# Performance work log

Measured on AMD Instinct MI355X. Metric: run time of the kernel, lower is better.

The kernel has to match this reference:

```python
import jax, jax.numpy as jnp
import numpy as np

D_MODEL = 256
NHEAD = 8
HEAD_DIM = D_MODEL // NHEAD
EPS_ATTN = 1e-6
EPS_LN = 1e-5


def _layernorm(x, g, b):
    mu = jnp.mean(x, axis=-1, keepdims=True)
    var = jnp.mean(jnp.square(x - mu), axis=-1, keepdims=True)
    return (x - mu) * jax.lax.rsqrt(var + EPS_LN) * g + b


def _embed_rotary(t, cos, sin):
    # t, cos, sin: [N, L, C]; interleaved pair rotation as in RoFPE.embed_rotary
    t2 = jnp.stack([-t[..., 1::2], t[..., ::2]], axis=-1).reshape(t.shape)
    return t * cos + t2 * sin


def setup_inputs() -> dict:
    key = jax.random.key(0)
    ks = jax.random.split(key, 12)
    N, L, S, C = 4, 4800, 4800, D_MODEL
    w = lambda k, shp: jax.random.normal(k, shp, dtype=jnp.float32) * 0.05
    return {
        "x": jax.random.normal(ks[0], (N, L, C), dtype=jnp.float32),
        "source": jax.random.normal(ks[1], (N, S, C), dtype=jnp.float32),
        "x_pe": jax.random.normal(ks[2], (N, L, C, 2), dtype=jnp.float32),
        "source_pe": jax.random.normal(ks[3], (N, S, C, 2), dtype=jnp.float32),
        "Wq": w(ks[4], (C, C)),
        "Wk": w(ks[5], (C, C)),
        "Wv": w(ks[6], (C, C)),
        "Wm": w(ks[7], (C, C)),
        "W1": w(ks[8], (2 * C, 2 * C)),
        "W2": w(ks[9], (C, 2 * C)),
        "g1": jnp.ones((C,), dtype=jnp.float32),
        "b1": jnp.zeros((C,), dtype=jnp.float32),
        "g2": jnp.ones((C,), dtype=jnp.float32),
        "b2": jnp.zeros((C,), dtype=jnp.float32),
    }


def reference(x, source, x_pe, source_pe, Wq, Wk, Wv, Wm, W1, W2, g1, b1, g2, b2):
    bs, L, C = x.shape
    H, D = NHEAD, HEAD_DIM
    # projections (nn.Linear: y = x @ W.T)
    q = x @ Wq.T
    k = source @ Wk.T
    v = source @ Wv.T
    # inline rotary PE
    q = _embed_rotary(q, x_pe[..., 0], x_pe[..., 1]).reshape(bs, L, H, D)
    k = _embed_rotary(k, source_pe[..., 0], source_pe[..., 1]).reshape(bs, -1, H, D)
    v = v.reshape(bs, -1, H, D)
    # LoFTR linear attention: phi(x) = elu(x) + 1
    Q = jax.nn.elu(q) + 1.0
    K = jax.nn.elu(k) + 1.0
    v_len = v.shape[1]
    vals = v / v_len
    KV = jnp.einsum("nshd,nshv->nhdv", K, vals)          # [N,H,D,D]
    Z = 1.0 / (jnp.einsum("nlhd,nhd->nlh", Q, K.sum(axis=1)) + EPS_ATTN)
    msg = jnp.einsum("nlhd,nhdv,nlh->nlhv", Q, KV, Z) * v_len  # [N,L,H,D]
    # merge + norm1
    msg = msg.reshape(bs, L, H * D) @ Wm.T
    msg = _layernorm(msg, g1, b1)
    # concat-MLP + norm2 + residual
    h = jnp.concatenate([x, msg], axis=-1)               # [N,L,2C]
    h = jax.nn.relu(h @ W1.T) @ W2.T
    h = _layernorm(h, g2, b2)
    return x + h
```

## Files before the change

### kernel.cpp

```cpp
#include <hip/hip_runtime.h>
#include <hip/hip_bf16.h>
#include <math.h>

#define NROWS 19200
#define SLEN  4800
#define KV_CHUNKS 50
#define KV_SC     96

typedef unsigned short ushort_t;
typedef __attribute__((ext_vector_type(8))) short bf16x8;
typedef __attribute__((ext_vector_type(4))) float f32x4;
typedef __attribute__((ext_vector_type(8))) unsigned short ushort8;

__device__ __forceinline__ float bf2f(ushort_t u) {
  union { unsigned int i; float f; } x; x.i = ((unsigned int)u) << 16; return x.f;
}
__device__ __forceinline__ ushort_t f2bf(float f) {
  __hip_bfloat16 h = __float2bfloat16(f);
  union { __hip_bfloat16 h; ushort_t u; } x; x.h = h; return x.u;
}

#define GLOAD16(g, l) __builtin_amdgcn_global_load_lds( \
    (const __attribute__((address_space(1))) unsigned int*)(g), \
    (__attribute__((address_space(3))) unsigned int*)(l), 16, 0, 0)

template <int EPI, bool CONCAT>
__device__ __forceinline__ void gemmT_body(
    const ushort_t* __restrict__ A0, const ushort_t* __restrict__ A1,
    const ushort_t* __restrict__ W, ushort_t* __restrict__ outp,
    int Nn, int K, int bm, int bn, char* smem) {
  const int tid = threadIdx.x;
  const int wave = tid >> 6, lane = tid & 63;
  const int wm = (wave >> 1) * 64, wn = (wave & 1) * 64;
  const int l15 = lane & 15, l4 = lane >> 4;

  f32x4 acc[4][4];
#pragma unroll
  for (int i = 0; i < 4; ++i)
#pragma unroll
    for (int j = 0; j < 4; ++j) acc[i][j] = (f32x4){0.f, 0.f, 0.f, 0.f};

  for (int k0 = 0; k0 < K; k0 += 64) {
    const ushort_t* Asrc;
    int ka;
    if (CONCAT) { Asrc = (k0 < 256) ? A0 : A1; ka = k0 & 255; }
    else        { Asrc = A0; ka = k0; }
#pragma unroll
    for (int c = 0; c < 4; ++c) {
      int ch = c * 4 + wave;
      int o = ch * 1024 + lane * 16;
      int row = o >> 7, g = (o >> 4) & 7;
      const ushort_t* sp =
          Asrc + (size_t)(bm + row) * 256 + ka + ((g ^ (row & 7)) << 3);
      GLOAD16(sp, smem + ch * 1024);
    }
#pragma unroll
    for (int c = 0; c < 4; ++c) {
      int ch = c * 4 + wave;
      int o = ch * 1024 + lane * 16;
      int row = o >> 7, g = (o >> 4) & 7;
      const ushort_t* sp =
          W + (size_t)(bn + row) * K + k0 + ((g ^ (row & 7)) << 3);
      GLOAD16(sp, smem + 16384 + ch * 1024);
    }
    __syncthreads();
#pragma unroll
    for (int kc = 0; kc < 2; ++kc) {
      bf16x8 af[4], bfr[4];
#pragma unroll
      for (int mi = 0; mi < 4; ++mi) {
        int r = wm + mi * 16 + l15;
        int G = kc * 4 + l4;
        af[mi] = *(const bf16x8*)(smem + r * 128 + ((G ^ (r & 7)) << 4));
      }
#pragma unroll
      for (int ni = 0; ni < 4; ++ni) {
        int r = wn + ni * 16 + l15;
        int G = kc * 4 + l4;
        bfr[ni] = *(const bf16x8*)(smem + 16384 + r * 128 +
                                   ((G ^ (r & 7)) << 4));
      }
#pragma unroll
      for (int mi = 0; mi < 4; ++mi)
#pragma unroll
        for (int ni = 0; ni < 4; ++ni)
          acc[mi][ni] = __builtin_amdgcn_mfma_f32_16x16x32_bf16(
              af[mi], bfr[ni], acc[mi][ni], 0, 0, 0);
    }
    __syncthreads();
  }

  ushort_t* st = (ushort_t*)smem;
#pragma unroll
  for (int mi = 0; mi < 4; ++mi)
#pragma unroll
    for (int ni = 0; ni < 4; ++ni)
#pragma unroll
      for (int j = 0; j < 4; ++j) {
        int trow = wm + mi * 16 + l4 * 4 + j;
        int tcol = wn + ni * 16 + l15;
        float v = acc[mi][ni][j];
        if (EPI == 3) v = fmaxf(v, 0.f);
        st[trow * 140 + tcol] = f2bf(v);
      }
  __syncthreads();
#pragma unroll
  for (int c = 0; c < 8; ++c) {
    int ch = c * 256 + tid;
    int row = ch >> 4, g = ch & 15;
    ushort8 u = *(const ushort8*)&st[row * 140 + g * 8];
    *(ushort8*)&outp[(size_t)(bm + row) * Nn + bn + g * 8] = u;
  }
}

__global__ __launch_bounds__(256) void qkv_fused(
    const ushort_t* __restrict__ xb, const ushort_t* __restrict__ srcb,
    const ushort_t* __restrict__ Wqb, const ushort_t* __restrict__ Wkb,
    const ushort_t* __restrict__ Wvb,
    ushort_t* __restrict__ Q, ushort_t* __restrict__ Kb,
    ushort_t* __restrict__ Vb) {
  extern __shared__ char smem[];
  int b = blockIdx.x;
  const int which = b < 300 ? 0 : (b < 600 ? 1 : 2);
  b -= which * 300;
  const int bm = (b >> 1) * 128, bn = (b & 1) * 128;
  const ushort_t* A = (which == 0) ? xb : srcb;
  const ushort_t* W = (which == 0) ? Wqb : (which == 1 ? Wkb : Wvb);
  ushort_t* o = (which == 0) ? Q : (which == 1 ? Kb : Vb);
  gemmT_body<0, false>(A, nullptr, W, o, 256, 256, bm, bn, smem);
}

__global__ __launch_bounds__(256) void mlp1_kernel(
    const ushort_t* __restrict__ xb, const ushort_t* __restrict__ msgln,
    const ushort_t* __restrict__ W1b, ushort_t* __restrict__ h1) {
  extern __shared__ char smem[];
  const int bm = (blockIdx.x >> 2) * 128, bn = (blockIdx.x & 3) * 128;
  gemmT_body<3, true>(xb, msgln, W1b, h1, 512, 512, bm, bn, smem);
}

template <int KDIM, bool RESID, bool OUTBF>
__global__ __launch_bounds__(256) void gemm_ln_kernel(
    const ushort_t* __restrict__ A, const ushort_t* __restrict__ W,
    const float* __restrict__ g, const float* __restrict__ bb,
    const float* __restrict__ resid, void* __restrict__ outp) {
  __shared__ char As[32 * 128];
  __shared__ char Bs[256 * 128];
  __shared__ float partS[4][32];
  __shared__ float partQ[4][32];
  __shared__ float gS[256], bS[256];

  const int tid = threadIdx.x;
  const int wave = tid >> 6, lane = tid & 63;
  const int l15 = lane & 15, l4 = lane >> 4;
  const int bm = blockIdx.x * 32;

  gS[tid] = g[tid];
  bS[tid] = bb[tid];

  f32x4 acc[2][4];
#pragma unroll
  for (int i = 0; i < 2; ++i)
#pragma unroll
    for (int j = 0; j < 4; ++j) acc[i][j] = (f32x4){0.f, 0.f, 0.f, 0.f};

  for (int k0 = 0; k0 < KDIM; k0 += 64) {
    {
      int row = tid >> 3, gch = tid & 7;
      const ushort_t* src =
          A + (size_t)(bm + row) * KDIM + k0 + ((gch ^ (row & 7)) << 3);
      GLOAD16(src, As + tid * 16);
    }
#pragma unroll
    for (int c = 0; c < 8; ++c) {
      int ch = c * 256 + tid;
      int row = ch >> 3, gch = ch & 7;
      const ushort_t* src =
          W + (size_t)row * KDIM + k0 + ((gch ^ (row & 7)) << 3);
      GLOAD16(src, Bs + ch * 16);
    }
    __syncthreads();
#pragma unroll
    for (int kc = 0; kc < 2; ++kc) {
      bf16x8 af[2], bfr[4];
#pragma unroll
      for (int mi = 0; mi < 2; ++mi) {
        int r = mi * 16 + l15;
        int G = kc * 4 + l4;
        af[mi] = *(const bf16x8*)(As + r * 128 + ((G ^ (r & 7)) << 4));
      }
#pragma unroll
      for (int ni = 0; ni < 4; ++ni) {
        int r = wave * 64 + ni * 16 + l15;
        int G = kc * 4 + l4;
        bfr[ni] = *(const bf16x8*)(Bs + r * 128 + ((G ^ (r & 7)) << 4));
      }
#pragma unroll
      for (int mi = 0; mi < 2; ++mi)
#pragma unroll
        for (int ni = 0; ni < 4; ++ni)
          acc[mi][ni] = __builtin_amdgcn_mfma_f32_16x16x32_bf16(
              af[mi], bfr[ni], acc[mi][ni], 0, 0, 0);
    }
    __syncthreads();
  }

#pragma unroll
  for (int mi = 0; mi < 2; ++mi)
#pragma unroll
    for (int j = 0; j < 4; ++j) {
      float s = acc[mi][0][j] + acc[mi][1][j] + acc[mi][2][j] + acc[mi][3][j];
      float q = acc[mi][0][j] * acc[mi][0][j] + acc[mi][1][j] * acc[mi][1][j] +
                acc[mi][2][j] * acc[mi][2][j] + acc[mi][3][j] * acc[mi][3][j];
#pragma unroll
      for (int m = 1; m < 16; m <<= 1) {
        s += __shfl_xor(s, m);
        q += __shfl_xor(q, m);
      }
      if (l15 == 0) {
        int row = mi * 16 + l4 * 4 + j;
        partS[wave][row] = s;
        partQ[wave][row] = q;
      }
    }
  __syncthreads();

  float mu[2][4], rsv[2][4];
#pragma unroll
  for (int mi = 0; mi < 2; ++mi)
#pragma unroll
    for (int j = 0; j < 4; ++j) {
      int row = mi * 16 + l4 * 4 + j;
      float s = partS[0][row] + partS[1][row] + partS[2][row] + partS[3][row];
      float q2 = partQ[0][row] + partQ[1][row] + partQ[2][row] + partQ[3][row];
      float m_ = s * (1.f / 256.f);
      float var = q2 * (1.f / 256.f) - m_ * m_;
      mu[mi][j] = m_;
      rsv[mi][j] = rsqrtf(var + 1e-5f);
    }

#pragma unroll
  for (int mi = 0; mi < 2; ++mi)
#pragma unroll
    for (int ni = 0; ni < 4; ++ni)
#pragma unroll
      for (int j = 0; j < 4; ++j) {
        int row = mi * 16 + l4 * 4 + j;
        int col = wave * 64 + ni * 16 + l15;
        float v = (acc[mi][ni][j] - mu[mi][j]) * rsv[mi][j] * gS[col] + bS[col];
        size_t gr = (size_t)(bm + row);
        if (RESID) v += resid[gr * 256 + col];
        if (OUTBF)
          ((ushort_t*)outp)[gr * 256 + col] = f2bf(v);
        else
          ((float*)outp)[gr * 256 + col] = v;
      }
}

__global__ __launch_bounds__(256) void kv_partial(
    const ushort_t* __restrict__ Kb, const ushort_t* __restrict__ Vb,
    const float* __restrict__ s_pe,
    float* __restrict__ kvp, float* __restrict__ ksp) {
  __shared__ float bufK[32][32];
  __shared__ float bufV[32][32];
  const int b = blockIdx.x;
  const int ch = b % KV_CHUNKS;
  const int nh = b / KV_CHUNKS;
  const int h = nh & 7, n = nh >> 3;
  const int tid = threadIdx.x;
  const int d = tid >> 3, vb = (tid & 7) * 4;
  const int half = tid >> 7, t = tid & 127;
  const int srow = t >> 2, seg = (t & 3) * 8;
  const int segS = (seg + 8 * (srow & 3)) & 31;
  float a0 = 0.f, a1 = 0.f, a2 = 0.f, a3 = 0.f, ks = 0.f;
  const size_t base = (size_t)n * SLEN * 256 + (size_t)h * 32;
  const int s0 = ch * KV_SC;
  for (int s = s0; s < s0 + KV_SC; s += 32) {
    __syncthreads();
    const size_t eoff = base + (size_t)(s + srow) * 256 + seg;
    ushort8 u = *(const ushort8*)((half ? Vb : Kb) + eoff);
    float v[8];
#pragma unroll
    for (int i = 0; i < 8; ++i) v[i] = bf2f((ushort_t)u[i]);
    if (!half) {
      const float4* pp = (const float4*)&s_pe[eoff * 2];
      float4 p0 = pp[0], p1 = pp[1], p2 = pp[2], p3 = pp[3];
      float r[8];
      r[0] = v[0] * p0.x - v[1] * p0.y; r[1] = v[1] * p0.z + v[0] * p0.w;
      r[2] = v[2] * p1.x - v[3] * p1.y; r[3] = v[3] * p1.z + v[2] * p1.w;
      r[4] = v[4] * p2.x - v[5] * p2.y; r[5] = v[5] * p2.z + v[4] * p2.w;
      r[6] = v[6] * p3.x - v[7] * p3.y; r[7] = v[7] * p3.z + v[6] * p3.w;
#pragma unroll
      for (int i = 0; i < 8; ++i)
        v[i] = r[i] > 0.f ? r[i] + 1.f : __expf(r[i]);
    }
    float* dst = half ? &bufV[srow][segS] : &bufK[srow][segS];
    *(float4*)dst = (float4){v[0], v[1], v[2], v[3]};
    *(float4*)(dst + 4) = (float4){v[4], v[5], v[6], v[7]};
    __syncthreads();
#pragma unroll
    for (int ss = 0; ss < 32; ++ss) {
      int rot = 8 * (ss & 3);
      float kd = bufK[ss][(d + rot) & 31];
      float4 vv = *(const float4*)&bufV[ss][(vb + rot) & 31];
      a0 += kd * vv.x; a1 += kd * vv.y; a2 += kd * vv.z; a3 += kd * vv.w;
      ks += kd;
    }
  }
  float* kv = &kvp[(size_t)b * 1024 + d * 32 + vb];
  kv[0] = a0; kv[1] = a1; kv[2] = a2; kv[3] = a3;
  if ((tid & 7) == 0) ksp[(size_t)b * 32 + d] = ks;
}

__global__ __launch_bounds__(256) void kv_reduce(
    const float* __restrict__ kvp, const float* __restrict__ ksp,
    float* __restrict__ KV, float* __restrict__ Ksum) {
  const int nh = blockIdx.x;
  const int tid = threadIdx.x;
  for (int e = tid; e < 1024; e += 256) {
    float s = 0.f;
    for (int p = 0; p < KV_CHUNKS; ++p)
      s += kvp[(size_t)(nh * KV_CHUNKS + p) * 1024 + e];
    KV[(size_t)nh * 1024 + e] = s;
  }
  if (tid < 32) {
    float s = 0.f;
    for (int p = 0; p < KV_CHUNKS; ++p)
      s += ksp[(size_t)(nh * KV_CHUNKS + p) * 32 + tid];
    Ksum[nh * 32 + tid] = s;
  }
}

__global__ __launch_bounds__(256) void msg_kernel(
    const ushort_t* __restrict__ Qb, const float* __restrict__ x_pe,
    const float* __restrict__ KV, const float* __restrict__ Ksum,
    ushort_t* __restrict__ msg) {
  __shared__ float Qs[8][256];
  __shared__ float Ks[8][32];
  const int b = blockIdx.x;
  const int r0 = b * 8;
  const int n = r0 / SLEN;
  const int tid = threadIdx.x;
  Ks[tid >> 5][tid & 31] = Ksum[(n * 8 + (tid >> 5)) * 32 + (tid & 31)];
  {
    int rr = tid >> 5, cc = (tid & 31) * 8;
    const size_t eoff = (size_t)(r0 + rr) * 256 + cc;
    const ushort8 u = *(const ushort8*)&Qb[eoff];
    const float4* pp = (const float4*)&x_pe[eoff * 2];
    float4 p0 = pp[0], p1 = pp[1], p2 = pp[2], p3 = pp[3];
    float v[8];
#pragma unroll
    for (int i = 0; i < 8; ++i) v[i] = bf2f((ushort_t)u[i]);
    float r[8];
    r[0] = v[0] * p0.x - v[1] * p0.y; r[1] = v[1] * p0.z + v[0] * p0.w;
    r[2] = v[2] * p1.x - v[3] * p1.y; r[3] = v[3] * p1.z + v[2] * p1.w;
    r[4] = v[4] * p2.x - v[5] * p2.y; r[5] = v[5] * p2.z + v[4] * p2.w;
    r[6] = v[6] * p3.x - v[7] * p3.y; r[7] = v[7] * p3.z + v[6] * p3.w;
#pragma unroll
    for (int i = 0; i < 8; ++i)
      Qs[rr][cc + i] = r[i] > 0.f ? r[i] + 1.f : __expf(r[i]);
  }
  __syncthreads();
  const int h = tid >> 5, v = tid & 31;
  const float* kvh = &KV[(size_t)(n * 8 + h) * 1024 + v];
  float kvc[32];
#pragma unroll
  for (int d = 0; d < 32; ++d) kvc[d] = kvh[d * 32];
#pragma unroll
  for (int rr = 0; rr < 8; ++rr) {
    float z = 0.f, m = 0.f;
#pragma unroll
    for (int d = 0; d < 32; ++d) {
      float qd = Qs[rr][h * 32 + d];
      z += qd * Ks[h][d];
      m += qd * kvc[d];
    }
    z = 1.0f / (z + 1e-6f);
    msg[(size_t)(r0 + rr) * 256 + h * 32 + v] = f2bf(m * z);
  }
}

__global__ __launch_bounds__(256) void conv_all(
    const float* __restrict__ x, const float* __restrict__ src,
    const float* w0, const float* w1, const float* w2, const float* w3,
    const float* w4, const float* w5,
    ushort_t* __restrict__ xo, ushort_t* __restrict__ so,
    ushort_t* o0, ushort_t* o1, ushort_t* o2, ushort_t* o3, ushort_t* o4,
    ushort_t* o5) {
  int blk = blockIdx.x;
  if (blk < 4800) {
    const float* s; ushort_t* d;
    if (blk < 2400) { s = x; d = xo; } else { s = src; d = so; blk -= 2400; }
    size_t o = ((size_t)blk * 256 + threadIdx.x) * 8;
    float4 v0 = *(const float4*)&s[o];
    float4 v1 = *(const float4*)&s[o + 4];
    ushort8 u = {f2bf(v0.x), f2bf(v0.y), f2bf(v0.z), f2bf(v0.w),
                 f2bf(v1.x), f2bf(v1.y), f2bf(v1.z), f2bf(v1.w)};
    *(ushort8*)&d[o] = u;
  } else {
    int e = ((blk - 4800) * 256 + threadIdx.x) * 4;
    const float* s; ushort_t* d; int off;
    if      (e < 65536)  { s = w0; d = o0; off = e; }
    else if (e < 131072) { s = w1; d = o1; off = e - 65536; }
    else if (e < 196608) { s = w2; d = o2; off = e - 131072; }
    else if (e < 262144) { s = w3; d = o3; off = e - 196608; }
    else if (e < 524288) { s = w4; d = o4; off = e - 262144; }
    else                 { s = w5; d = o5; off = e - 524288; }
    float4 v = *(const float4*)&s[off];
    ushort4 u = make_ushort4(f2bf(v.x), f2bf(v.y), f2bf(v.z), f2bf(v.w));
    *(ushort4*)&d[off] = u;
  }
}

extern "C" void kernel_launch(void* const* d_in, const int* in_sizes, int n_in,
                              void* d_out, int out_size, void* d_ws,
                              size_t ws_size, hipStream_t stream) {
  const float* x    = (const float*)d_in[0];
  const float* src  = (const float*)d_in[1];
  const float* x_pe = (const float*)d_in[2];
  const float* s_pe = (const float*)d_in[3];
  const float* Wq = (const float*)d_in[4];
  const float* Wk = (const float*)d_in[5];
  const float* Wv = (const float*)d_in[6];
  const float* Wm = (const float*)d_in[7];
  const float* W1 = (const float*)d_in[8];
  const float* W2 = (const float*)d_in[9];
  const float* g1 = (const float*)d_in[10];
  const float* b1 = (const float*)d_in[11];
  const float* g2 = (const float*)d_in[12];
  const float* b2 = (const float*)d_in[13];
  float* out = (float*)d_out;

  const size_t R = (size_t)NROWS * 256;
  ushort_t* xb    = (ushort_t*)d_ws;
  ushort_t* srcb  = xb + R;
  ushort_t* Qb    = srcb + R;
  ushort_t* Kb    = Qb + R;
  ushort_t* Vb    = Kb + R;
  ushort_t* msgln = Vb + R;
  ushort_t* Wqb   = msgln + R;
  ushort_t* Wkb   = Wqb + 65536;
  ushort_t* Wvb   = Wkb + 65536;
  ushort_t* Wmb   = Wvb + 65536;
  ushort_t* W1b   = Wmb + 65536;
  ushort_t* W2b   = W1b + 262144;
  float* kvp      = (float*)(W2b + 131072);
  float* ksp      = kvp + 1638400;
  float* KVb      = ksp + 51200;
  float* Ksum     = KVb + 32768;
  ushort_t* msgb = srcb;
  ushort_t* h1   = Kb;

  dim3 blk(256);
  conv_all<<<5440, blk, 0, stream>>>(x, src, Wq, Wk, Wv, Wm, W1, W2,
                                     xb, srcb, Wqb, Wkb, Wvb, Wmb, W1b, W2b);
  qkv_fused<<<900, blk, 35840, stream>>>(xb, srcb, Wqb, Wkb, Wvb, Qb, Kb, Vb);
  kv_partial<<<1600, blk, 0, stream>>>(Kb, Vb, s_pe, kvp, ksp);
  kv_reduce<<<32, blk, 0, stream>>>(kvp, ksp, KVb, Ksum);
  msg_kernel<<<2400, blk, 0, stream>>>(Qb, x_pe, KVb, Ksum, msgb);
  gemm_ln_kernel<256, false, true><<<600, blk, 0, stream>>>(
      msgb, Wmb, g1, b1, nullptr, msgln);
  mlp1_kernel<<<600, blk, 35840, stream>>>(xb, msgln, W1b, h1);
  gemm_ln_kernel<512, true, false><<<600, blk, 0, stream>>>(
      h1, W2b, g2, b2, x, out);
}
```

Baseline: 135.0 us.

## Load fp32 activations directly into GEMMs, drop separate bf16 conversion pass

Result: slower. 154.0 us (+14.1%).

```diff
diff --git a/kernel.cpp b/kernel.cpp
--- a/kernel.cpp
+++ b/kernel.cpp
@@ -25,8 +25,8 @@
     (__attribute__((address_space(3))) unsigned int*)(l), 16, 0, 0)
 
 template <int EPI, bool CONCAT>
-__device__ __forceinline__ void gemmT_body(
-    const ushort_t* __restrict__ A0, const ushort_t* __restrict__ A1,
+__device__ __forceinline__ void gemmF_body(
+    const float* __restrict__ A0, const float* __restrict__ A1,
     const ushort_t* __restrict__ W, ushort_t* __restrict__ outp,
     int Nn, int K, int bm, int bn, char* smem) {
   const int tid = threadIdx.x;
@@ -41,17 +41,17 @@
     for (int j = 0; j < 4; ++j) acc[i][j] = (f32x4){0.f, 0.f, 0.f, 0.f};
 
   for (int k0 = 0; k0 < K; k0 += 64) {
-    const ushort_t* Asrc;
+    const float* Asrc;
     int ka;
     if (CONCAT) { Asrc = (k0 < 256) ? A0 : A1; ka = k0 & 255; }
     else        { Asrc = A0; ka = k0; }
 #pragma unroll
-    for (int c = 0; c < 4; ++c) {
+    for (int c = 0; c < 8; ++c) {
       int ch = c * 4 + wave;
-      int o = ch * 1024 + lane * 16;
-      int row = o >> 7, g = (o >> 4) & 7;
-      const ushort_t* sp =
-          Asrc + (size_t)(bm + row) * 256 + ka + ((g ^ (row & 7)) << 3);
+      int row = ch * 4 + (lane >> 4);
+      int g = lane & 15;
+      int gsrc = g ^ ((row & 7) << 1);
+      const float* sp = Asrc + (size_t)(bm + row) * 256 + ka + gsrc * 4;
       GLOAD16(sp, smem + ch * 1024);
     }
 #pragma unroll
@@ -61,7 +61,7 @@
       int row = o >> 7, g = (o >> 4) & 7;
       const ushort_t* sp =
           W + (size_t)(bn + row) * K + k0 + ((g ^ (row & 7)) << 3);
-      GLOAD16(sp, smem + 16384 + ch * 1024);
+      GLOAD16(sp, smem + 32768 + ch * 1024);
     }
     __syncthreads();
 #pragma unroll
@@ -70,14 +70,22 @@
 #pragma unroll
       for (int mi = 0; mi < 4; ++mi) {
         int r = wm + mi * 16 + l15;
-        int G = kc * 4 + l4;
-        af[mi] = *(const bf16x8*)(smem + r * 128 + ((G ^ (r & 7)) << 4));
+        int G0 = (kc * 8 + l4 * 2) ^ ((r & 7) << 1);
+        const float* fp = (const float*)(smem + r * 256 + G0 * 16);
+        f32x4 a0 = *(const f32x4*)fp;
+        f32x4 a1 = *(const f32x4*)(fp + 4);
+        bf16x8 t;
+        t[0] = (short)f2bf(a0[0]); t[1] = (short)f2bf(a0[1]);
+        t[2] = (short)f2bf(a0[2]); t[3] = (short)f2bf(a0[3]);
+        t[4] = (short)f2bf(a1[0]); t[5] = (short)f2bf(a1[1]);
+        t[6] = (short)f2bf(a1[2]); t[7] = (short)f2bf(a1[3]);
+        af[mi] = t;
       }
 #pragma unroll
       for (int ni = 0; ni < 4; ++ni) {
         int r = wn + ni * 16 + l15;
         int G = kc * 4 + l4;
-        bfr[ni] = *(const bf16x8*)(smem + 16384 + r * 128 +
+        bfr[ni] = *(const bf16x8*)(smem + 32768 + r * 128 +
                                    ((G ^ (r & 7)) << 4));
       }
 #pragma unroll
@@ -114,7 +122,7 @@
 }
 
 __global__ __launch_bounds__(256) void qkv_fused(
-    const ushort_t* __restrict__ xb, const ushort_t* __restrict__ srcb,
+    const float* __restrict__ x, const float* __restrict__ src,
     const ushort_t* __restrict__ Wqb, const ushort_t* __restrict__ Wkb,
     const ushort_t* __restrict__ Wvb,
     ushort_t* __restrict__ Q, ushort_t* __restrict__ Kb,
@@ -124,18 +132,18 @@
   const int which = b < 300 ? 0 : (b < 600 ? 1 : 2);
   b -= which * 300;
   const int bm = (b >> 1) * 128, bn = (b & 1) * 128;
-  const ushort_t* A = (which == 0) ? xb : srcb;
+  const float* A = (which == 0) ? x : src;
   const ushort_t* W = (which == 0) ? Wqb : (which == 1 ? Wkb : Wvb);
   ushort_t* o = (which == 0) ? Q : (which == 1 ? Kb : Vb);
-  gemmT_body<0, false>(A, nullptr, W, o, 256, 256, bm, bn, smem);
+  gemmF_body<0, false>(A, nullptr, W, o, 256, 256, bm, bn, smem);
 }
 
 __global__ __launch_bounds__(256) void mlp1_kernel(
-    const ushort_t* __restrict__ xb, const ushort_t* __restrict__ msgln,
+    const float* __restrict__ x, const float* __restrict__ msgln,
     const ushort_t* __restrict__ W1b, ushort_t* __restrict__ h1) {
   extern __shared__ char smem[];
   const int bm = (blockIdx.x >> 2) * 128, bn = (blockIdx.x & 3) * 128;
-  gemmT_body<3, true>(xb, msgln, W1b, h1, 512, 512, bm, bn, smem);
+  gemmF_body<3, true>(x, msgln, W1b, h1, 512, 512, bm, bn, smem);
 }
 
 template <int KDIM, bool RESID, bool OUTBF>
@@ -379,36 +387,22 @@
   }
 }
 
-__global__ __launch_bounds__(256) void conv_all(
-    const float* __restrict__ x, const float* __restrict__ src,
+__global__ __launch_bounds__(256) void conv_w(
     const float* w0, const float* w1, const float* w2, const float* w3,
     const float* w4, const float* w5,
-    ushort_t* __restrict__ xo, ushort_t* __restrict__ so,
     ushort_t* o0, ushort_t* o1, ushort_t* o2, ushort_t* o3, ushort_t* o4,
     ushort_t* o5) {
-  int blk = blockIdx.x;
-  if (blk < 4800) {
-    const float* s; ushort_t* d;
-    if (blk < 2400) { s = x; d = xo; } else { s = src; d = so; blk -= 2400; }
-    size_t o = ((size_t)blk * 256 + threadIdx.x) * 8;
-    float4 v0 = *(const float4*)&s[o];
-    float4 v1 = *(const float4*)&s[o + 4];
-    ushort8 u = {f2bf(v0.x), f2bf(v0.y), f2bf(v0.z), f2bf(v0.w),
-                 f2bf(v1.x), f2bf(v1.y), f2bf(v1.z), f2bf(v1.w)};
-    *(ushort8*)&d[o] = u;
-  } else {
-    int e = ((blk - 4800) * 256 + threadIdx.x) * 4;
-    const float* s; ushort_t* d; int off;
-    if      (e < 65536)  { s = w0; d = o0; off = e; }
-    else if (e < 131072) { s = w1; d = o1; off = e - 65536; }
-    else if (e < 196608) { s = w2; d = o2; off = e - 131072; }
-    else if (e < 262144) { s = w3; d = o3; off = e - 196608; }
-    else if (e < 524288) { s = w4; d = o4; off = e - 262144; }
-    else                 { s = w5; d = o5; off = e - 524288; }
-    float4 v = *(const float4*)&s[off];
-    ushort4 u = make_ushort4(f2bf(v.x), f2bf(v.y), f2bf(v.z), f2bf(v.w));
-    *(ushort4*)&d[off] = u;
-  }
+  int e = (blockIdx.x * 256 + threadIdx.x) * 4;
+  const float* s; ushort_t* d; int off;
+  if      (e < 65536)  { s = w0; d = o0; off = e; }
+  else if (e < 131072) { s = w1; d = o1; off = e - 65536; }
+  else if (e < 196608) { s = w2; d = o2; off = e - 131072; }
+  else if (e < 262144) { s = w3; d = o3; off = e - 196608; }
+  else if (e < 524288) { s = w4; d = o4; off = e - 262144; }
+  else                 { s = w5; d = o5; off = e - 524288; }
+  float4 v = *(const float4*)&s[off];
+  ushort4 u = make_ushort4(f2bf(v.x), f2bf(v.y), f2bf(v.z), f2bf(v.w));
+  *(ushort4*)&d[off] = u;
 }
 
 extern "C" void kernel_launch(void* const* d_in, const int* in_sizes, int n_in,
@@ -431,13 +425,12 @@
   float* out = (float*)d_out;
 
   const size_t R = (size_t)NROWS * 256;
-  ushort_t* xb    = (ushort_t*)d_ws;
-  ushort_t* srcb  = xb + R;
-  ushort_t* Qb    = srcb + R;
+  ushort_t* Qb    = (ushort_t*)d_ws;
   ushort_t* Kb    = Qb + R;
   ushort_t* Vb    = Kb + R;
-  ushort_t* msgln = Vb + R;
-  ushort_t* Wqb   = msgln + R;
+  ushort_t* msgb  = Vb + R;
+  float*    msgln = (float*)(msgb + R);
+  ushort_t* Wqb   = (ushort_t*)(msgln + R);
   ushort_t* Wkb   = Wqb + 65536;
   ushort_t* Wvb   = Wkb + 65536;
   ushort_t* Wmb   = Wvb + 65536;
@@ -447,19 +440,18 @@
   float* ksp      = kvp + 1638400;
   float* KVb      = ksp + 51200;
   float* Ksum     = KVb + 32768;
-  ushort_t* msgb = srcb;
-  ushort_t* h1   = Kb;
+  ushort_t* h1    = Kb;
 
   dim3 blk(256);
-  conv_all<<<5440, blk, 0, stream>>>(x, src, Wq, Wk, Wv, Wm, W1, W2,
-                                     xb, srcb, Wqb, Wkb, Wvb, Wmb, W1b, W2b);
-  qkv_fused<<<900, blk, 35840, stream>>>(xb, srcb, Wqb, Wkb, Wvb, Qb, Kb, Vb);
+  conv_w<<<640, blk, 0, stream>>>(Wq, Wk, Wv, Wm, W1, W2,
+                                  Wqb, Wkb, Wvb, Wmb, W1b, W2b);
+  qkv_fused<<<900, blk, 49152, stream>>>(x, src, Wqb, Wkb, Wvb, Qb, Kb, Vb);
   kv_partial<<<1600, blk, 0, stream>>>(Kb, Vb, s_pe, kvp, ksp);
   kv_reduce<<<32, blk, 0, stream>>>(kvp, ksp, KVb, Ksum);
   msg_kernel<<<2400, blk, 0, stream>>>(Qb, x_pe, KVb, Ksum, msgb);
-  gemm_ln_kernel<256, false, true><<<600, blk, 0, stream>>>(
+  gemm_ln_kernel<256, false, false><<<600, blk, 0, stream>>>(
       msgb, Wmb, g1, b1, nullptr, msgln);
-  mlp1_kernel<<<600, blk, 35840, stream>>>(xb, msgln, W1b, h1);
+  mlp1_kernel<<<600, blk, 49152, stream>>>(x, msgln, W1b, h1);
   gemm_ln_kernel<512, true, false><<<600, blk, 0, stream>>>(
       h1, W2b, g2, b2, x, out);
 }
```

## Fuse linear-attention message computation into merge GEMM with LayerNorm

Applied to the files above, without the earlier changes.

Result: no change. 132.9 us (-1.6%).

```diff
diff --git a/kernel.cpp b/kernel.cpp
--- a/kernel.cpp
+++ b/kernel.cpp
@@ -136,6 +136,175 @@
   extern __shared__ char smem[];
   const int bm = (blockIdx.x >> 2) * 128, bn = (blockIdx.x & 3) * 128;
   gemmT_body<3, true>(xb, msgln, W1b, h1, 512, 512, bm, bn, smem);
+}
+
+__global__ __launch_bounds__(256) void msg_merge_ln(
+    const ushort_t* __restrict__ Qb, const float* __restrict__ x_pe,
+    const float* __restrict__ KV, const float* __restrict__ Ksum,
+    const ushort_t* __restrict__ Wm,
+    const float* __restrict__ g, const float* __restrict__ bb,
+    ushort_t* __restrict__ msgln) {
+  __shared__ char mem[33024];
+  __shared__ char Bs[256 * 128];
+  __shared__ float Ks[8][32];
+  __shared__ float partS[4][32];
+  __shared__ float partQ[4][32];
+  __shared__ float gS[256], bS[256];
+
+  const int tid = threadIdx.x;
+  const int wave = tid >> 6, lane = tid & 63;
+  const int l15 = lane & 15, l4 = lane >> 4;
+  const int bm = blockIdx.x * 32;
+  const int n = bm / SLEN;
+
+  gS[tid] = g[tid];
+  bS[tid] = bb[tid];
+  Ks[tid >> 5][tid & 31] = Ksum[(n * 8 + (tid >> 5)) * 32 + (tid & 31)];
+
+  float* phiQ = (float*)mem;
+#pragma unroll
+  for (int p = 0; p < 4; ++p) {
+    int rr = p * 8 + (tid >> 5), cc = (tid & 31) * 8;
+    const size_t eoff = (size_t)(bm + rr) * 256 + cc;
+    const ushort8 uq = *(const ushort8*)&Qb[eoff];
+    const float4* pp = (const float4*)&x_pe[eoff * 2];
+    float4 p0 = pp[0], p1 = pp[1], p2 = pp[2], p3 = pp[3];
+    float v[8];
+#pragma unroll
+    for (int i = 0; i < 8; ++i) v[i] = bf2f((ushort_t)uq[i]);
+    float r[8];
+    r[0] = v[0] * p0.x - v[1] * p0.y; r[1] = v[1] * p0.z + v[0] * p0.w;
+    r[2] = v[2] * p1.x - v[3] * p1.y; r[3] = v[3] * p1.z + v[2] * p1.w;
+    r[4] = v[4] * p2.x - v[5] * p2.y; r[5] = v[5] * p2.z + v[4] * p2.w;
+    r[6] = v[6] * p3.x - v[7] * p3.y; r[7] = v[7] * p3.z + v[6] * p3.w;
+#pragma unroll
+    for (int i = 0; i < 8; ++i)
+      v[i] = r[i] > 0.f ? r[i] + 1.f : __expf(r[i]);
+    float* dst = &phiQ[rr * 258 + cc];
+#pragma unroll
+    for (int i = 0; i < 4; ++i)
+      *(float2*)(dst + 2 * i) = (float2){v[2 * i], v[2 * i + 1]};
+  }
+  __syncthreads();
+
+  const int h = tid >> 5, v = tid & 31;
+  const float* kvh = &KV[(size_t)(n * 8 + h) * 1024 + v];
+  float kvc[32];
+#pragma unroll
+  for (int d = 0; d < 32; ++d) kvc[d] = kvh[d * 32];
+  ushort_t msge[32];
+#pragma unroll
+  for (int rr = 0; rr < 32; ++rr) {
+    float z = 0.f, m = 0.f;
+#pragma unroll
+    for (int d = 0; d < 32; ++d) {
+      float qd = phiQ[rr * 258 + h * 32 + d];
+      z += qd * Ks[h][d];
+      m += qd * kvc[d];
+    }
+    z = 1.0f / (z + 1e-6f);
+    msge[rr] = f2bf(m * z);
+  }
+  __syncthreads();
+
+  ushort_t* As = (ushort_t*)mem;
+  const int col = tid;
+  const int gi0 = col >> 3, cb = col & 7;
+#pragma unroll
+  for (int rr = 0; rr < 32; ++rr) {
+    int gis = (gi0 & ~7) | ((gi0 & 7) ^ (rr & 7));
+    As[rr * 256 + gis * 8 + cb] = msge[rr];
+  }
+  __syncthreads();
+
+  f32x4 acc[2][4];
+#pragma unroll
+  for (int i = 0; i < 2; ++i)
+#pragma unroll
+    for (int j = 0; j < 4; ++j) acc[i][j] = (f32x4){0.f, 0.f, 0.f, 0.f};
+
+  for (int k0 = 0; k0 < 256; k0 += 64) {
+#pragma unroll
+    for (int c = 0; c < 8; ++c) {
+      int ch = c * 256 + tid;
+      int row = ch >> 3, gch = ch & 7;
+      const ushort_t* src =
+          Wm + (size_t)row * 256 + k0 + ((gch ^ (row & 7)) << 3);
+      GLOAD16(src, Bs + ch * 16);
+    }
+    __syncthreads();
+#pragma unroll
+    for (int kc = 0; kc < 2; ++kc) {
+      bf16x8 af[2], bfr[4];
+#pragma unroll
+      for (int mi = 0; mi < 2; ++mi) {
+        int r = mi * 16 + l15;
+        int gi = (k0 >> 3) + kc * 4 + l4;
+        int gis = (gi & ~7) | ((gi & 7) ^ (r & 7));
+        af[mi] = *(const bf16x8*)(As + r * 256 + gis * 8);
+      }
+#pragma unroll
+      for (int ni = 0; ni < 4; ++ni) {
+        int r = wave * 64 + ni * 16 + l15;
+        int G = kc * 4 + l4;
+        bfr[ni] = *(const bf16x8*)(Bs + r * 128 + ((G ^ (r & 7)) << 4));
+      }
+#pragma unroll
+      for (int mi = 0; mi < 2; ++mi)
+#pragma unroll
+        for (int ni = 0; ni < 4; ++ni)
+          acc[mi][ni] = __builtin_amdgcn_mfma_f32_16x16x32_bf16(
+              af[mi], bfr[ni], acc[mi][ni], 0, 0, 0);
+    }
+    __syncthreads();
+  }
+
+#pragma unroll
+  for (int mi = 0; mi < 2; ++mi)
+#pragma unroll
+    for (int j = 0; j < 4; ++j) {
+      float s = acc[mi][0][j] + acc[mi][1][j] + acc[mi][2][j] + acc[mi][3][j];
+      float q = acc[mi][0][j] * acc[mi][0][j] + acc[mi][1][j] * acc[mi][1][j] +
+                acc[mi][2][j] * acc[mi][2][j] + acc[mi][3][j] * acc[mi][3][j];
+#pragma unroll
+      for (int m = 1; m < 16; m <<= 1) {
+        s += __shfl_xor(s, m);
+        q += __shfl_xor(q, m);
+      }
+      if (l15 == 0) {
+        int row = mi * 16 + l4 * 4 + j;
+        partS[wave][row] = s;
+        partQ[wave][row] = q;
+      }
+    }
+  __syncthreads();
+
+  float mu[2][4], rsv[2][4];
+#pragma unroll
+  for (int mi = 0; mi < 2; ++mi)
+#pragma unroll
+    for (int j = 0; j < 4; ++j) {
+      int row = mi * 16 + l4 * 4 + j;
+      float s = partS[0][row] + partS[1][row] + partS[2][row] + partS[3][row];
+      float q2 = partQ[0][row] + partQ[1][row] + partQ[2][row] + partQ[3][row];
+      float m_ = s * (1.f / 256.f);
+      float var = q2 * (1.f / 256.f) - m_ * m_;
+      mu[mi][j] = m_;
+      rsv[mi][j] = rsqrtf(var + 1e-5f);
+    }
+
+#pragma unroll
+  for (int mi = 0; mi < 2; ++mi)
+#pragma unroll
+    for (int ni = 0; ni < 4; ++ni)
+#pragma unroll
+      for (int j = 0; j < 4; ++j) {
+        int row = mi * 16 + l4 * 4 + j;
+        int col2 = wave * 64 + ni * 16 + l15;
+        float vv = (acc[mi][ni][j] - mu[mi][j]) * rsv[mi][j] * gS[col2] +
+                   bS[col2];
+        msgln[(size_t)(bm + row) * 256 + col2] = f2bf(vv);
+      }
 }
 
 template <int KDIM, bool RESID, bool OUTBF>
@@ -327,55 +496,6 @@
     for (int p = 0; p < KV_CHUNKS; ++p)
       s += ksp[(size_t)(nh * KV_CHUNKS + p) * 32 + tid];
     Ksum[nh * 32 + tid] = s;
-  }
-}
-
-__global__ __launch_bounds__(256) void msg_kernel(
-    const ushort_t* __restrict__ Qb, const float* __restrict__ x_pe,
-    const float* __restrict__ KV, const float* __restrict__ Ksum,
-    ushort_t* __restrict__ msg) {
-  __shared__ float Qs[8][256];
-  __shared__ float Ks[8][32];
-  const int b = blockIdx.x;
-  const int r0 = b * 8;
-  const int n = r0 / SLEN;
-  const int tid = threadIdx.x;
-  Ks[tid >> 5][tid & 31] = Ksum[(n * 8 + (tid >> 5)) * 32 + (tid & 31)];
-  {
-    int rr = tid >> 5, cc = (tid & 31) * 8;
-    const size_t eoff = (size_t)(r0 + rr) * 256 + cc;
-    const ushort8 u = *(const ushort8*)&Qb[eoff];
-    const float4* pp = (const float4*)&x_pe[eoff * 2];
-    float4 p0 = pp[0], p1 = pp[1], p2 = pp[2], p3 = pp[3];
-    float v[8];
-#pragma unroll
-    for (int i = 0; i < 8; ++i) v[i] = bf2f((ushort_t)u[i]);
-    float r[8];
-    r[0] = v[0] * p0.x - v[1] * p0.y; r[1] = v[1] * p0.z + v[0] * p0.w;
-    r[2] = v[2] * p1.x - v[3] * p1.y; r[3] = v[3] * p1.z + v[2] * p1.w;
-    r[4] = v[4] * p2.x - v[5] * p2.y; r[5] = v[5] * p2.z + v[4] * p2.w;
-    r[6] = v[6] * p3.x - v[7] * p3.y; r[7] = v[7] * p3.z + v[6] * p3.w;
-#pragma unroll
-    for (int i = 0; i < 8; ++i)
-      Qs[rr][cc + i] = r[i] > 0.f ? r[i] + 1.f : __expf(r[i]);
-  }
-  __syncthreads();
-  const int h = tid >> 5, v = tid & 31;
-  const float* kvh = &KV[(size_t)(n * 8 + h) * 1024 + v];
-  float kvc[32];
-#pragma unroll
-  for (int d = 0; d < 32; ++d) kvc[d] = kvh[d * 32];
-#pragma unroll
-  for (int rr = 0; rr < 8; ++rr) {
-    float z = 0.f, m = 0.f;
-#pragma unroll
-    for (int d = 0; d < 32; ++d) {
-      float qd = Qs[rr][h * 32 + d];
-      z += qd * Ks[h][d];
-      m += qd * kvc[d];
-    }
-    z = 1.0f / (z + 1e-6f);
-    msg[(size_t)(r0 + rr) * 256 + h * 32 + v] = f2bf(m * z);
   }
 }
 
@@ -447,7 +567,6 @@
   float* ksp      = kvp + 1638400;
   float* KVb      = ksp + 51200;
   float* Ksum     = KVb + 32768;
-  ushort_t* msgb = srcb;
   ushort_t* h1   = Kb;
 
   dim3 blk(256);
@@ -456,9 +575,8 @@
   qkv_fused<<<900, blk, 35840, stream>>>(xb, srcb, Wqb, Wkb, Wvb, Qb, Kb, Vb);
   kv_partial<<<1600, blk, 0, stream>>>(Kb, Vb, s_pe, kvp, ksp);
   kv_reduce<<<32, blk, 0, stream>>>(kvp, ksp, KVb, Ksum);
-  msg_kernel<<<2400, blk, 0, stream>>>(Qb, x_pe, KVb, Ksum, msgb);
-  gemm_ln_kernel<256, false, true><<<600, blk, 0, stream>>>(
-      msgb, Wmb, g1, b1, nullptr, msgln);
+  msg_merge_ln<<<600, blk, 0, stream>>>(Qb, x_pe, KVb, Ksum, Wmb, g1, b1,
+                                        msgln);
   mlp1_kernel<<<600, blk, 35840, stream>>>(xb, msgln, W1b, h1);
   gemm_ln_kernel<512, true, false><<<600, blk, 0, stream>>>(
       h1, W2b, g2, b2, x, out);
```
